# Performance work log

Hardware: AMD Instinct MI355X
Metric: run time of the kernel (lower is better)

## Reference

```python
import jax, jax.numpy as jnp
import numpy as np

NUM_HEADS = 16
KEY_DIM = 64
NUM_FEATURES = 256
D_MODEL = NUM_HEADS * KEY_DIM
EPS = 1e-6


def softmax_kernel(data, proj):
    # data: [..., N, D], proj: [D, F]
    # Faithful to source: ratio uses proj.shape[0] (=D), matching the TF code.
    data_normalizer = 1.0 / jnp.sqrt(jnp.sqrt(jnp.asarray(data.shape[-1], data.dtype)))
    ratio = 1.0 / jnp.sqrt(jnp.asarray(proj.shape[0], data.dtype))
    data = data_normalizer * data
    data_dash = jnp.einsum('...nd,df->...nf', data, proj)
    diag = jnp.sum(jnp.square(data), axis=-1, keepdims=True)  # [..., N, 1]
    return ratio * (jnp.exp(data_dash - diag / 2.0) + EPS)


def setup_inputs() -> dict:
    key = jax.random.key(0)
    ks = jax.random.split(key, 12)
    B, N = 4, 4096
    s = 1.0 / np.sqrt(D_MODEL)
    inp = {
        'queries': jax.random.normal(ks[0], (B, N, D_MODEL), jnp.float32),
        'keys': jax.random.normal(ks[1], (B, N, D_MODEL), jnp.float32),
        'Wq': jax.random.normal(ks[2], (D_MODEL, D_MODEL), jnp.float32) * s,
        'bq': jnp.zeros((D_MODEL,), jnp.float32),
        'Wk': jax.random.normal(ks[3], (D_MODEL, D_MODEL), jnp.float32) * s,
        'bk': jnp.zeros((D_MODEL,), jnp.float32),
        'Wv': jax.random.normal(ks[4], (D_MODEL, D_MODEL), jnp.float32) * s,
        'bv': jnp.zeros((D_MODEL,), jnp.float32),
        'Wo': jax.random.normal(ks[5], (D_MODEL, D_MODEL), jnp.float32) * s,
        'bo': jnp.zeros((D_MODEL,), jnp.float32),
        # GlorotNormal for [KEY_DIM, NUM_FEATURES]
        'proj': jax.random.normal(ks[6], (KEY_DIM, NUM_FEATURES), jnp.float32)
                * np.sqrt(2.0 / (KEY_DIM + NUM_FEATURES)),
    }
    return inp


def reference(queries, keys, Wq, bq, Wk, bk, Wv, bv, Wo, bo, proj):
    # Original code uses x = queries for q, k, v (self-attention); keys arg unused.
    x = queries
    B, N, _ = x.shape
    H, D = NUM_HEADS, KEY_DIM

    def split_heads(t):
        return t.reshape(B, N, H, D).transpose(0, 2, 1, 3)  # [B,H,N,D]

    q = split_heads(x @ Wq + bq)
    k = split_heads(x @ Wk + bk)
    v = split_heads(x @ Wv + bv)

    q_prime = softmax_kernel(q, proj)  # [B,H,N,F]
    k_prime = softmax_kernel(k, proj)  # [B,H,N,F]

    kv = jnp.einsum('bhnf,bhnd->bhfd', k_prime, v)        # [B,H,F,D]
    qkv = jnp.einsum('bhnf,bhfd->bhnd', q_prime, kv)       # [B,H,N,D]
    k_sum = jnp.sum(k_prime, axis=2)                        # [B,H,F]
    norm = jnp.einsum('bhnf,bhf->bhn', q_prime, k_sum) + EPS
    qkv = qkv / norm[..., None]

    out = qkv.transpose(0, 2, 1, 3).reshape(B, N, H * D)    # [B,N,d_model]
    return out @ Wo + bo
```

## Files before the change

### kernel.cpp

```cpp
#include <hip/hip_runtime.h>

typedef __attribute__((ext_vector_type(8))) short short8;
typedef __attribute__((ext_vector_type(4))) float f32x4;

#define MFMA16 __builtin_amdgcn_mfma_f32_16x16x32_bf16

#define GLOAD16(gp, lp) __builtin_amdgcn_global_load_lds(                      \
    (const __attribute__((address_space(1))) void*)(gp),                       \
    (__attribute__((address_space(3))) void*)(lp), 16, 0, 0)

__device__ __forceinline__ unsigned short f2bf(float f) {
  unsigned int u = __float_as_uint(f);
  unsigned int r = u + 0x7fffu + ((u >> 16) & 1u);
  return (unsigned short)(r >> 16);
}
__device__ __forceinline__ float bf2f(unsigned short h) {
  return __uint_as_float(((unsigned int)h) << 16);
}

__global__ __launch_bounds__(256) void cast_x_kernel(
    const float* __restrict__ in, unsigned short* __restrict__ out, int n4) {
  int i = blockIdx.x * 256 + threadIdx.x;
  if (i >= n4) return;
  float4 v = reinterpret_cast<const float4*>(in)[i];
  ushort4 o;
  o.x = f2bf(v.x); o.y = f2bf(v.y); o.z = f2bf(v.z); o.w = f2bf(v.w);
  reinterpret_cast<ushort4*>(out)[i] = o;
}

__global__ __launch_bounds__(256) void tcast_f32_kernel(
    const float* __restrict__ in, unsigned short* __restrict__ out, int R, int C) {
  __shared__ float t[64][65];
  int c0 = blockIdx.x * 64, r0 = blockIdx.y * 64;
  int tx = threadIdx.x, ty = threadIdx.y;
#pragma unroll
  for (int i = 0; i < 16; ++i)
    t[ty + 4 * i][tx] = in[(size_t)(r0 + ty + 4 * i) * C + c0 + tx];
  __syncthreads();
#pragma unroll
  for (int i = 0; i < 16; ++i)
    out[(size_t)(c0 + ty + 4 * i) * R + r0 + tx] = f2bf(t[tx][ty + 4 * i]);
}

__global__ __launch_bounds__(256) void t_bf16_kernel(
    const unsigned short* __restrict__ in, unsigned short* __restrict__ out, int R, int C) {
  __shared__ unsigned short t[64][66];
  size_t base = (size_t)blockIdx.z * (size_t)R * (size_t)C;
  int c0 = blockIdx.x * 64, r0 = blockIdx.y * 64;
  int tx = threadIdx.x, ty = threadIdx.y;
#pragma unroll
  for (int i = 0; i < 16; ++i)
    t[ty + 4 * i][tx] = in[base + (size_t)(r0 + ty + 4 * i) * C + c0 + tx];
  __syncthreads();
#pragma unroll
  for (int i = 0; i < 16; ++i)
    out[base + (size_t)(c0 + ty + 4 * i) * R + r0 + tx] = t[tx][ty + 4 * i];
}

template <int OUTF>
__global__ __launch_bounds__(256) void gemm_bt_kernel(
    const unsigned short* __restrict__ A,
    const unsigned short* W0, const unsigned short* W1, const unsigned short* W2,
    const float* b0, const float* b1, const float* b2,
    void* o0, void* o1, void* o2) {
  constexpr int KD = 1024, ND = 1024;
  const unsigned short* W = W0; const float* bias = b0; void* op = o0;
  if (blockIdx.z == 1) { W = W1; bias = b1; op = o1; }
  else if (blockIdx.z == 2) { W = W2; bias = b2; op = o2; }

  __shared__ unsigned short lsA[128 * 32];
  __shared__ unsigned short lsB[128 * 32];
  int tid = threadIdx.x;
  int w = tid >> 6, lane = tid & 63;
  int m0 = blockIdx.x * 128, n0 = blockIdx.y * 128;
  int wm = (w >> 1) * 64, wn = (w & 1) * 64;

  int srow0 = (w * 2 + 0) * 16 + (lane >> 2);
  int srow1 = (w * 2 + 1) * 16 + (lane >> 2);
  int scol = (lane & 3) * 8;
  const unsigned short* gA0 = A + (size_t)(m0 + srow0) * KD + scol;
  const unsigned short* gA1 = A + (size_t)(m0 + srow1) * KD + scol;
  const unsigned short* gB0 = W + (size_t)(n0 + srow0) * KD + scol;
  const unsigned short* gB1 = W + (size_t)(n0 + srow1) * KD + scol;
  unsigned short* lA0 = &lsA[(w * 2 + 0) * 512];
  unsigned short* lA1 = &lsA[(w * 2 + 1) * 512];
  unsigned short* lB0 = &lsB[(w * 2 + 0) * 512];
  unsigned short* lB1 = &lsB[(w * 2 + 1) * 512];

  f32x4 acc[4][4];
#pragma unroll
  for (int fm = 0; fm < 4; ++fm)
#pragma unroll
    for (int fn = 0; fn < 4; ++fn) acc[fm][fn] = (f32x4){0.f, 0.f, 0.f, 0.f};

  for (int kt = 0; kt < KD; kt += 32) {
    GLOAD16(gA0 + kt, lA0);
    GLOAD16(gA1 + kt, lA1);
    GLOAD16(gB0 + kt, lB0);
    GLOAD16(gB1 + kt, lB1);
    __syncthreads();
    short8 af[4], bfr[4];
#pragma unroll
    for (int fm = 0; fm < 4; ++fm)
      af[fm] = *reinterpret_cast<const short8*>(
          &lsA[(wm + fm * 16 + (lane & 15)) * 32 + (lane >> 4) * 8]);
#pragma unroll
    for (int fn = 0; fn < 4; ++fn)
      bfr[fn] = *reinterpret_cast<const short8*>(
          &lsB[(wn + fn * 16 + (lane & 15)) * 32 + (lane >> 4) * 8]);
#pragma unroll
    for (int fm = 0; fm < 4; ++fm)
#pragma unroll
      for (int fn = 0; fn < 4; ++fn)
        acc[fm][fn] = MFMA16(af[fm], bfr[fn], acc[fm][fn], 0, 0, 0);
    __syncthreads();
  }

#pragma unroll
  for (int fn = 0; fn < 4; ++fn) {
    int col = n0 + wn + fn * 16 + (lane & 15);
    float bv = bias[col];
#pragma unroll
    for (int fm = 0; fm < 4; ++fm) {
#pragma unroll
      for (int j = 0; j < 4; ++j) {
        int row = m0 + wm + fm * 16 + (lane >> 4) * 4 + j;
        float v = acc[fm][fn][j] + bv;
        if (OUTF)
          reinterpret_cast<float*>(op)[(size_t)row * ND + col] = v;
        else
          reinterpret_cast<unsigned short*>(op)[(size_t)row * ND + col] = f2bf(v);
      }
    }
  }
}

__global__ __launch_bounds__(256) void kv_fused_kernel(
    const unsigned short* __restrict__ K, const unsigned short* __restrict__ PT,
    const unsigned short* __restrict__ VT,
    float* __restrict__ kvp, float* __restrict__ ksp) {
  __shared__ unsigned short kp[256 * 40];
  int s = blockIdx.x, bh = blockIdx.y, b = bh >> 4, h = bh & 15;
  int tid = threadIdx.x, w = tid >> 6, lane = tid & 63;
  int lo = lane & 15, hi = lane >> 4;
  int f0w = w * 64;

  f32x4 acck[4][4];
#pragma unroll
  for (int fm = 0; fm < 4; ++fm)
#pragma unroll
    for (int fn = 0; fn < 4; ++fn) acck[fm][fn] = (f32x4){0.f, 0.f, 0.f, 0.f};
  float ks[4] = {0.f, 0.f, 0.f, 0.f};

  for (int c = 0; c < 32; ++c) {
    int n0 = s * 1024 + c * 32;
    const unsigned short* Ab = K + (size_t)(b * 4096 + n0) * 1024 + h * 64;
    short8 af[2][2];
    float dp[2] = {0.f, 0.f};
#pragma unroll
    for (int fm = 0; fm < 2; ++fm)
#pragma unroll
      for (int kt = 0; kt < 2; ++kt) {
        af[fm][kt] = *reinterpret_cast<const short8*>(
            Ab + (size_t)(fm * 16 + lo) * 1024 + kt * 32 + hi * 8);
#pragma unroll
        for (int j = 0; j < 8; ++j) {
          float qv = bf2f((unsigned short)af[fm][kt][j]);
          dp[fm] += qv * qv;
        }
      }
#pragma unroll
    for (int fm = 0; fm < 2; ++fm) {
      dp[fm] += __shfl_xor(dp[fm], 16);
      dp[fm] += __shfl_xor(dp[fm], 32);
    }
    f32x4 accf[2][4];
#pragma unroll
    for (int fm = 0; fm < 2; ++fm)
#pragma unroll
      for (int fn = 0; fn < 4; ++fn) accf[fm][fn] = (f32x4){0.f, 0.f, 0.f, 0.f};
#pragma unroll
    for (int fn = 0; fn < 4; ++fn) {
      int f = f0w + fn * 16 + lo;
      short8 pb0 = *reinterpret_cast<const short8*>(PT + (size_t)f * 64 + hi * 8);
      short8 pb1 = *reinterpret_cast<const short8*>(PT + (size_t)f * 64 + 32 + hi * 8);
      accf[0][fn] = MFMA16(af[0][0], pb0, accf[0][fn], 0, 0, 0);
      accf[0][fn] = MFMA16(af[0][1], pb1, accf[0][fn], 0, 0, 0);
      accf[1][fn] = MFMA16(af[1][0], pb0, accf[1][fn], 0, 0, 0);
      accf[1][fn] = MFMA16(af[1][1], pb1, accf[1][fn], 0, 0, 0);
    }
#pragma unroll
    for (int fm = 0; fm < 2; ++fm)
#pragma unroll
      for (int fn = 0; fn < 4; ++fn)
#pragma unroll
        for (int j = 0; j < 4; ++j) {
          float dg = __shfl(dp[fm], hi * 4 + j);
          float v = 0.125f *
                    (__expf(0.35355339059327373f * accf[fm][fn][j] - 0.0625f * dg) + 1e-6f);
          ks[fn] += v;
          kp[(f0w + fn * 16 + lo) * 40 + fm * 16 + hi * 4 + j] = f2bf(v);
        }
    __syncthreads();
    short8 a2[4], b2[4];
#pragma unroll
    for (int fm = 0; fm < 4; ++fm)
      a2[fm] = *reinterpret_cast<const short8*>(&kp[(f0w + fm * 16 + lo) * 40 + hi * 8]);
#pragma unroll
    for (int fn = 0; fn < 4; ++fn)
      b2[fn] = *reinterpret_cast<const short8*>(
          VT + (size_t)(bh * 64 + fn * 16 + lo) * 4096 + n0 + hi * 8);
#pragma unroll
    for (int fm = 0; fm < 4; ++fm)
#pragma unroll
      for (int fn = 0; fn < 4; ++fn)
        acck[fm][fn] = MFMA16(a2[fm], b2[fn], acck[fm][fn], 0, 0, 0);
    __syncthreads();
  }
#pragma unroll
  for (int fn = 0; fn < 4; ++fn) {
    float v = ks[fn];
    v += __shfl_xor(v, 16);
    v += __shfl_xor(v, 32);
    if (hi == 0)
      ksp[(size_t)(s * 64 + bh) * 256 + f0w + fn * 16 + lo] = v;
  }
#pragma unroll
  for (int fm = 0; fm < 4; ++fm)
#pragma unroll
    for (int fn = 0; fn < 4; ++fn)
#pragma unroll
      for (int j = 0; j < 4; ++j)
        kvp[((size_t)(s * 64 + bh) * 256 + f0w + fm * 16 + hi * 4 + j) * 64 + fn * 16 + lo] =
            acck[fm][fn][j];
}

__global__ __launch_bounds__(256) void kvred_kernel(
    const float* __restrict__ kvp, const float* __restrict__ ksp,
    unsigned short* __restrict__ kvT, float* __restrict__ ksum) {
  int bh = blockIdx.x, tid = threadIdx.x;
  for (int i = tid; i < 64 * 256; i += 256) {
    int f = i >> 6, d = i & 63;
    float sum = 0.f;
#pragma unroll
    for (int s = 0; s < 4; ++s)
      sum += kvp[((size_t)(s * 64 + bh) * 256 + f) * 64 + d];
    kvT[(size_t)(bh * 64 + d) * 256 + f] = f2bf(sum);
  }
  {
    float t = 0.f;
#pragma unroll
    for (int s = 0; s < 4; ++s) t += ksp[(size_t)(s * 64 + bh) * 256 + tid];
    ksum[bh * 256 + tid] = t;
  }
}

__global__ __launch_bounds__(256) void qkv_fused_kernel(
    const unsigned short* __restrict__ Q, const unsigned short* __restrict__ PT,
    const unsigned short* __restrict__ KVT, const float* __restrict__ KSUM,
    unsigned short* __restrict__ Y) {
  __shared__ unsigned short qp[128 * 256];
  int bh = blockIdx.y, b = bh >> 4, h = bh & 15;
  int t0 = blockIdx.x * 128;
  int tid = threadIdx.x, w = tid >> 6, lane = tid & 63;
  int lo = lane & 15, hi = lane >> 4;
  int r0 = w * 32;
  const unsigned short* Ab = Q + (size_t)(b * 4096 + t0 + r0) * 1024 + h * 64;

  float ksr[16];
#pragma unroll
  for (int fn = 0; fn < 16; ++fn) ksr[fn] = KSUM[bh * 256 + fn * 16 + lo];

  short8 af[2][2];
  float dp[2] = {0.f, 0.f};
#pragma unroll
  for (int fm = 0; fm < 2; ++fm)
#pragma unroll
    for (int kt = 0; kt < 2; ++kt) {
      af[fm][kt] = *reinterpret_cast<const short8*>(
          Ab + (size_t)(fm * 16 + lo) * 1024 + kt * 32 + hi * 8);
#pragma unroll
      for (int j = 0; j < 8; ++j) {
        float qv = bf2f((unsigned short)af[fm][kt][j]);
        dp[fm] += qv * qv;
      }
    }
#pragma unroll
  for (int fm = 0; fm < 2; ++fm) {
    dp[fm] += __shfl_xor(dp[fm], 16);
    dp[fm] += __shfl_xor(dp[fm], 32);
  }

  float np[2][4] = {{0.f, 0.f, 0.f, 0.f}, {0.f, 0.f, 0.f, 0.f}};
#pragma unroll
  for (int hf = 0; hf < 2; ++hf) {
    f32x4 accf[2][8];
#pragma unroll
    for (int fm = 0; fm < 2; ++fm)
#pragma unroll
      for (int fn = 0; fn < 8; ++fn) accf[fm][fn] = (f32x4){0.f, 0.f, 0.f, 0.f};
#pragma unroll
    for (int fn = 0; fn < 8; ++fn) {
      int f = (hf * 8 + fn) * 16 + lo;
      short8 pb0 = *reinterpret_cast<const short8*>(PT + (size_t)f * 64 + hi * 8);
      short8 pb1 = *reinterpret_cast<const short8*>(PT + (size_t)f * 64 + 32 + hi * 8);
      accf[0][fn] = MFMA16(af[0][0], pb0, accf[0][fn], 0, 0, 0);
      accf[0][fn] = MFMA16(af[0][1], pb1, accf[0][fn], 0, 0, 0);
      accf[1][fn] = MFMA16(af[1][0], pb0, accf[1][fn], 0, 0, 0);
      accf[1][fn] = MFMA16(af[1][1], pb1, accf[1][fn], 0, 0, 0);
    }
#pragma unroll
    for (int fm = 0; fm < 2; ++fm)
#pragma unroll
      for (int fn = 0; fn < 8; ++fn)
#pragma unroll
        for (int j = 0; j < 4; ++j) {
          float dg = __shfl(dp[fm], hi * 4 + j);
          float v = 0.125f *
                    (__expf(0.35355339059327373f * accf[fm][fn][j] - 0.0625f * dg) + 1e-6f);
          np[fm][j] += v * ksr[hf * 8 + fn];
          int row = r0 + fm * 16 + hi * 4 + j;
          int f = (hf * 8 + fn) * 16 + lo;
          int byt = (row * 512 + f * 2) ^ ((row & 7) << 4);
          *reinterpret_cast<unsigned short*>(reinterpret_cast<char*>(qp) + byt) = f2bf(v);
        }
  }
#pragma unroll
  for (int fm = 0; fm < 2; ++fm)
#pragma unroll
    for (int j = 0; j < 4; ++j) {
      np[fm][j] += __shfl_xor(np[fm][j], 1);
      np[fm][j] += __shfl_xor(np[fm][j], 2);
      np[fm][j] += __shfl_xor(np[fm][j], 4);
      np[fm][j] += __shfl_xor(np[fm][j], 8);
    }
  __syncthreads();
  f32x4 acco[2][4];
#pragma unroll
  for (int fm = 0; fm < 2; ++fm)
#pragma unroll
    for (int fn = 0; fn < 4; ++fn) acco[fm][fn] = (f32x4){0.f, 0.f, 0.f, 0.f};
#pragma unroll
  for (int kt2 = 0; kt2 < 8; ++kt2) {
    short8 a2[2], b2[4];
#pragma unroll
    for (int fm = 0; fm < 2; ++fm) {
      int row = r0 + fm * 16 + lo;
      int byt = (row * 512 + kt2 * 64 + hi * 16) ^ ((row & 7) << 4);
      a2[fm] = *reinterpret_cast<const short8*>(reinterpret_cast<char*>(qp) + byt);
    }
#pragma unroll
    for (int fn = 0; fn < 4; ++fn)
      b2[fn] = *reinterpret_cast<const short8*>(
          KVT + (size_t)(bh * 64 + fn * 16 + lo) * 256 + kt2 * 32 + hi * 8);
#pragma unroll
    for (int fm = 0; fm < 2; ++fm)
#pragma unroll
      for (int fn = 0; fn < 4; ++fn)
        acco[fm][fn] = MFMA16(a2[fm], b2[fn], acco[fm][fn], 0, 0, 0);
  }
#pragma unroll
  for (int fm = 0; fm < 2; ++fm)
#pragma unroll
    for (int j = 0; j < 4; ++j) {
      float nv = np[fm][j] + 1e-6f;
      int row = b * 4096 + t0 + r0 + fm * 16 + hi * 4 + j;
#pragma unroll
      for (int fn = 0; fn < 4; ++fn)
        Y[(size_t)row * 1024 + h * 64 + fn * 16 + lo] = f2bf(acco[fm][fn][j] / nv);
    }
}

extern "C" void kernel_launch(void* const* d_in, const int* in_sizes, int n_in,
                              void* d_out, int out_size, void* d_ws, size_t ws_size,
                              hipStream_t stream) {
  (void)in_sizes; (void)n_in; (void)out_size; (void)ws_size;
  const float* x    = (const float*)d_in[0];
  const float* Wq   = (const float*)d_in[2];
  const float* bq   = (const float*)d_in[3];
  const float* Wk   = (const float*)d_in[4];
  const float* bk   = (const float*)d_in[5];
  const float* Wv   = (const float*)d_in[6];
  const float* bv   = (const float*)d_in[7];
  const float* Wo   = (const float*)d_in[8];
  const float* bo   = (const float*)d_in[9];
  const float* proj = (const float*)d_in[10];
  float* out = (float*)d_out;

  constexpr size_t SZ_XB = (size_t)16384 * 1024 * 2;
  constexpr size_t SZ_W  = (size_t)1024 * 1024 * 2;
  constexpr size_t SZ_PT = (size_t)256 * 64 * 2;

  char* p = (char*)d_ws;
  size_t off = 0;
  char* a_xb  = p + off; off += SZ_XB;
  char* a_WqT = p + off; off += SZ_W;
  char* a_WkT = p + off; off += SZ_W;
  char* a_WvT = p + off; off += SZ_W;
  char* a_WoT = p + off; off += SZ_W;
  char* a_pT  = p + off; off += SZ_PT;
  char* a_qb  = p + off; off += SZ_XB;
  char* a_kb  = p + off; off += SZ_XB;

  char* a_kvp  = a_xb;
  char* a_ksp  = a_xb + (size_t)4 * 64 * 256 * 64 * 4;
  char* a_kvT  = a_ksp + (size_t)4 * 64 * 256 * 4;
  char* a_ksum = a_kvT + (size_t)64 * 64 * 256 * 2;
  char* a_y = a_kb;
  char* a_vb = (char*)d_out;
  char* a_vT = (char*)d_out + SZ_XB;

  dim3 tb(64, 4);

  cast_x_kernel<<<16384, 256, 0, stream>>>(x, (unsigned short*)a_xb, 16384 * 1024 / 4);
  tcast_f32_kernel<<<dim3(16, 16), tb, 0, stream>>>(Wq, (unsigned short*)a_WqT, 1024, 1024);
  tcast_f32_kernel<<<dim3(16, 16), tb, 0, stream>>>(Wk, (unsigned short*)a_WkT, 1024, 1024);
  tcast_f32_kernel<<<dim3(16, 16), tb, 0, stream>>>(Wv, (unsigned short*)a_WvT, 1024, 1024);
  tcast_f32_kernel<<<dim3(16, 16), tb, 0, stream>>>(Wo, (unsigned short*)a_WoT, 1024, 1024);
  tcast_f32_kernel<<<dim3(4, 1), tb, 0, stream>>>(proj, (unsigned short*)a_pT, 64, 256);

  gemm_bt_kernel<0><<<dim3(128, 8, 3), 256, 0, stream>>>(
      (unsigned short*)a_xb,
      (unsigned short*)a_WqT, (unsigned short*)a_WkT, (unsigned short*)a_WvT,
      bq, bk, bv, a_qb, a_kb, a_vb);

  t_bf16_kernel<<<dim3(16, 64, 4), tb, 0, stream>>>(
      (unsigned short*)a_vb, (unsigned short*)a_vT, 4096, 1024);

  kv_fused_kernel<<<dim3(4, 64), 256, 0, stream>>>(
      (unsigned short*)a_kb, (unsigned short*)a_pT, (unsigned short*)a_vT,
      (float*)a_kvp, (float*)a_ksp);
  kvred_kernel<<<64, 256, 0, stream>>>(
      (float*)a_kvp, (float*)a_ksp, (unsigned short*)a_kvT, (float*)a_ksum);

  qkv_fused_kernel<<<dim3(32, 64), 256, 0, stream>>>(
      (unsigned short*)a_qb, (unsigned short*)a_pT, (unsigned short*)a_kvT,
      (float*)a_ksum, (unsigned short*)a_y);

  gemm_bt_kernel<1><<<dim3(128, 8, 1), 256, 0, stream>>>(
      (unsigned short*)a_y,
      (unsigned short*)a_WoT, nullptr, nullptr,
      bo, nullptr, nullptr, out, nullptr, nullptr);
}
```

Measured before the change: 390.8 us.

## Split KV reduction over eight sequence chunks and drop redundant block barriers

The key-feature/value accumulation kernel now splits the sequence into 8 chunks per batch-head instead of 4. That doubles the block count to give the GPU more parallel work, and the reduction kernel now sums 8 partials. The projection fragments and V row pointers are hoisted out of the chunk loop. The __syncthreads barriers in both fused kernels are removed, since each wave only reads the LDS rows it wrote itself. Workspace for the partial sums and reduced outputs is moved to separate regions because the larger partial buffer now fills the reused x buffer.

```diff
diff --git a/kernel.cpp b/kernel.cpp
--- a/kernel.cpp
+++ b/kernel.cpp
@@ -145,6 +145,18 @@
   int lo = lane & 15, hi = lane >> 4;
   int f0w = w * 64;
 
+  short8 pb[4][2];
+#pragma unroll
+  for (int fn = 0; fn < 4; ++fn) {
+    int f = f0w + fn * 16 + lo;
+    pb[fn][0] = *reinterpret_cast<const short8*>(PT + (size_t)f * 64 + hi * 8);
+    pb[fn][1] = *reinterpret_cast<const short8*>(PT + (size_t)f * 64 + 32 + hi * 8);
+  }
+  const unsigned short* vbase[4];
+#pragma unroll
+  for (int fn = 0; fn < 4; ++fn)
+    vbase[fn] = VT + (size_t)(bh * 64 + fn * 16 + lo) * 4096;
+
   f32x4 acck[4][4];
 #pragma unroll
   for (int fm = 0; fm < 4; ++fm)
@@ -152,8 +164,8 @@
     for (int fn = 0; fn < 4; ++fn) acck[fm][fn] = (f32x4){0.f, 0.f, 0.f, 0.f};
   float ks[4] = {0.f, 0.f, 0.f, 0.f};
 
-  for (int c = 0; c < 32; ++c) {
-    int n0 = s * 1024 + c * 32;
+  for (int c = 0; c < 16; ++c) {
+    int n0 = s * 512 + c * 32;
     const unsigned short* Ab = K + (size_t)(b * 4096 + n0) * 1024 + h * 64;
     short8 af[2][2];
     float dp[2] = {0.f, 0.f};
@@ -181,13 +193,10 @@
       for (int fn = 0; fn < 4; ++fn) accf[fm][fn] = (f32x4){0.f, 0.f, 0.f, 0.f};
 #pragma unroll
     for (int fn = 0; fn < 4; ++fn) {
-      int f = f0w + fn * 16 + lo;
-      short8 pb0 = *reinterpret_cast<const short8*>(PT + (size_t)f * 64 + hi * 8);
-      short8 pb1 = *reinterpret_cast<const short8*>(PT + (size_t)f * 64 + 32 + hi * 8);
-      accf[0][fn] = MFMA16(af[0][0], pb0, accf[0][fn], 0, 0, 0);
-      accf[0][fn] = MFMA16(af[0][1], pb1, accf[0][fn], 0, 0, 0);
-      accf[1][fn] = MFMA16(af[1][0], pb0, accf[1][fn], 0, 0, 0);
-      accf[1][fn] = MFMA16(af[1][1], pb1, accf[1][fn], 0, 0, 0);
+      accf[0][fn] = MFMA16(af[0][0], pb[fn][0], accf[0][fn], 0, 0, 0);
+      accf[0][fn] = MFMA16(af[0][1], pb[fn][1], accf[0][fn], 0, 0, 0);
+      accf[1][fn] = MFMA16(af[1][0], pb[fn][0], accf[1][fn], 0, 0, 0);
+      accf[1][fn] = MFMA16(af[1][1], pb[fn][1], accf[1][fn], 0, 0, 0);
     }
 #pragma unroll
     for (int fm = 0; fm < 2; ++fm)
@@ -201,21 +210,18 @@
           ks[fn] += v;
           kp[(f0w + fn * 16 + lo) * 40 + fm * 16 + hi * 4 + j] = f2bf(v);
         }
-    __syncthreads();
     short8 a2[4], b2[4];
 #pragma unroll
     for (int fm = 0; fm < 4; ++fm)
       a2[fm] = *reinterpret_cast<const short8*>(&kp[(f0w + fm * 16 + lo) * 40 + hi * 8]);
 #pragma unroll
     for (int fn = 0; fn < 4; ++fn)
-      b2[fn] = *reinterpret_cast<const short8*>(
-          VT + (size_t)(bh * 64 + fn * 16 + lo) * 4096 + n0 + hi * 8);
+      b2[fn] = *reinterpret_cast<const short8*>(vbase[fn] + n0 + hi * 8);
 #pragma unroll
     for (int fm = 0; fm < 4; ++fm)
 #pragma unroll
       for (int fn = 0; fn < 4; ++fn)
         acck[fm][fn] = MFMA16(a2[fm], b2[fn], acck[fm][fn], 0, 0, 0);
-    __syncthreads();
   }
 #pragma unroll
   for (int fn = 0; fn < 4; ++fn) {
@@ -243,14 +249,14 @@
     int f = i >> 6, d = i & 63;
     float sum = 0.f;
 #pragma unroll
-    for (int s = 0; s < 4; ++s)
+    for (int s = 0; s < 8; ++s)
       sum += kvp[((size_t)(s * 64 + bh) * 256 + f) * 64 + d];
     kvT[(size_t)(bh * 64 + d) * 256 + f] = f2bf(sum);
   }
   {
     float t = 0.f;
 #pragma unroll
-    for (int s = 0; s < 4; ++s) t += ksp[(size_t)(s * 64 + bh) * 256 + tid];
+    for (int s = 0; s < 8; ++s) t += ksp[(size_t)(s * 64 + bh) * 256 + tid];
     ksum[bh * 256 + tid] = t;
   }
 }
@@ -334,7 +340,6 @@
       np[fm][j] += __shfl_xor(np[fm][j], 4);
       np[fm][j] += __shfl_xor(np[fm][j], 8);
     }
-  __syncthreads();
   f32x4 acco[2][4];
 #pragma unroll
   for (int fm = 0; fm < 2; ++fm)
@@ -401,11 +406,11 @@
   char* a_pT  = p + off; off += SZ_PT;
   char* a_qb  = p + off; off += SZ_XB;
   char* a_kb  = p + off; off += SZ_XB;
-
-  char* a_kvp  = a_xb;
-  char* a_ksp  = a_xb + (size_t)4 * 64 * 256 * 64 * 4;
-  char* a_kvT  = a_ksp + (size_t)4 * 64 * 256 * 4;
-  char* a_ksum = a_kvT + (size_t)64 * 64 * 256 * 2;
+  char* a_ksp  = p + off; off += (size_t)8 * 64 * 256 * 4;
+  char* a_kvT  = p + off; off += (size_t)64 * 64 * 256 * 2;
+  char* a_ksum = p + off; off += (size_t)64 * 256 * 4;
+
+  char* a_kvp = a_xb;
   char* a_y = a_kb;
   char* a_vb = (char*)d_out;
   char* a_vT = (char*)d_out + SZ_XB;
@@ -427,7 +432,7 @@
   t_bf16_kernel<<<dim3(16, 64, 4), tb, 0, stream>>>(
       (unsigned short*)a_vb, (unsigned short*)a_vT, 4096, 1024);
 
-  kv_fused_kernel<<<dim3(4, 64), 256, 0, stream>>>(
+  kv_fused_kernel<<<dim3(8, 64), 256, 0, stream>>>(
       (unsigned short*)a_kb, (unsigned short*)a_pT, (unsigned short*)a_vT,
       (float*)a_kvp, (float*)a_ksp);
   kvred_kernel<<<64, 256, 0, stream>>>(
```

After: 356.4 us. -8.8%, faster.
